# Performance work log

Measured on AMD Instinct MI355X. Metric: run time of the kernel, lower is better.

Reference implementation:

```python
import jax, jax.numpy as jnp
import numpy as np


def setup_inputs() -> dict:
    key = jax.random.key(0)
    k1, k2, k3 = jax.random.split(key, 3)
    B, S, E = 4, 8192, 1024
    x = jax.random.normal(k1, (B, S, E), dtype=jnp.float32)
    # torch nn.Linear weights have shape [out_features, in_features]
    W1 = jax.random.normal(k2, (3 * E, E), dtype=jnp.float32) * (1.0 / np.sqrt(E))
    W2 = jax.random.normal(k3, (E, E), dtype=jnp.float32) * (1.0 / np.sqrt(E))
    return {"x": x, "W1": W1, "W2": W2, "heads": 16}


def reference(x, W1, W2, heads):
    B, S, E = x.shape
    h = heads
    e = E // h
    # qkv projection: [B,S,3E] -> 'b s (n h e) -> n b h s e'
    qkv = (x @ W1.T).reshape(B, S, 3, h, e)
    qkv = jnp.transpose(qkv, (2, 0, 3, 1, 4))  # [3,B,h,S,e]
    q, k, v = qkv[0], qkv[1], qkv[2]
    # score: [B,h,e,e], softmax over last dim (c)
    score = jax.nn.softmax(jnp.einsum('bhnk,bhnc->bhkc', k / 4, v), axis=-1)
    # einsum 'bhnk,bhkc->bhnk': elementwise over k, sum over c
    attn = jax.nn.softmax(jnp.einsum('bhnk,bhkc->bhnk', q / 4, score), axis=-1)
    # 'b h s e -> b s (h e)' then linear_2
    out = jnp.transpose(attn, (0, 2, 1, 3)).reshape(B, S, E) @ W2.T
    return out
```

## Files before the change

kernel.cpp:

```cpp
#include <hip/hip_runtime.h>
#include <hip/hip_bf16.h>
#include <stdint.h>

static constexpr int MTOT = 32768;
static constexpr int KD   = 1024;
static constexpr int ND   = 1024;

static constexpr int BM = 256, BN = 256, BK = 64;
static constexpr int NT = KD / BK;
static constexpr int BUF_BYTES = 65536;
static constexpr int BOFF = 32768;
static constexpr int HALF = 16384;

typedef __bf16 bf16x8 __attribute__((ext_vector_type(8)));
typedef float  f32x4  __attribute__((ext_vector_type(4)));

__device__ __forceinline__ unsigned short f2bf_rne(float f) {
  union { float f; uint32_t u; } c; c.f = f;
  uint32_t u = c.u;
  return (unsigned short)((u + 0x7fffu + ((u >> 16) & 1u)) >> 16);
}

__global__ void cast_f32_to_bf16(const float* __restrict__ src,
                                 unsigned short* __restrict__ dst, int n4) {
  int idx = blockIdx.x * blockDim.x + threadIdx.x;
  int stride = gridDim.x * blockDim.x;
  for (int i = idx; i < n4; i += stride) {
    float4 v = reinterpret_cast<const float4*>(src)[i];
    ushort4 o;
    o.x = f2bf_rne(v.x); o.y = f2bf_rne(v.y);
    o.z = f2bf_rne(v.z); o.w = f2bf_rne(v.w);
    reinterpret_cast<ushort4*>(dst)[i] = o;
  }
}

__device__ __forceinline__ void gload_lds16(const void* g, void* lds) {
  __builtin_amdgcn_global_load_lds(
      (const __attribute__((address_space(1))) unsigned int*)g,
      (__attribute__((address_space(3))) unsigned int*)lds, 16, 0, 0);
}

template <int SOFTMAX>
__global__ __launch_bounds__(512, 2)
void gemm8(const unsigned short* __restrict__ A,
           const unsigned short* __restrict__ Bm,
           void* __restrict__ Cout) {
  extern __shared__ __align__(16) char ldsc[];

  const int tid  = threadIdx.x;
  const int lane = tid & 63;
  const int wid  = tid >> 6;
  const int wm = wid >> 2, wn = wid & 3;
  const int fr = lane & 15, fq = lane >> 4;

  const int bid0 = blockIdx.x;
  const int bid  = ((bid0 & 7) << 6) | (bid0 >> 3);
  const int brow = (bid >> 2) * BM;
  const int bcol = (bid & 3) * BN;

  const int srow  = tid >> 3;
  const int sslot = (tid & 7) ^ (srow & 7);
  const unsigned short* gA = A  + (size_t)(brow + srow) * KD + sslot * 8;
  const unsigned short* gB = Bm + (size_t)(bcol + srow) * KD + sslot * 8;

  f32x4  acc[8][4] = {};
  bf16x8 a0[4][2], a1[4][2], bA[2][2], bB[2][2];

  auto STAGE = [&](const unsigned short* g, int h, int kt, int b, int opOff) {
    const unsigned short* gu = g + (size_t)(h * 128) * KD + kt * BK;
    char* du = ldsc + b * BUF_BYTES + opOff + h * HALF + (wid << 10);
    gload_lds16(gu, du);
    gload_lds16(gu + (size_t)64 * KD, du + 8192);
  };

  auto rdA = [&](int b, bf16x8 (*dst)[2], int mBase) {
    const char* base = ldsc + b * BUF_BYTES + wm * HALF;
    #pragma unroll
    for (int mm = 0; mm < 4; ++mm) {
      const int r = (mBase + mm) * 16 + fr;
      #pragma unroll
      for (int ks = 0; ks < 2; ++ks)
        dst[mm][ks] = *(const bf16x8*)(base + (r << 7) +
                        ((ks * 64 + fq * 16) ^ ((r & 7) << 4)));
    }
  };
  auto rdB = [&](int b, int nBase, bf16x8 (*dst)[2]) {
    const char* base = ldsc + b * BUF_BYTES + BOFF + (wn >> 1) * HALF;
    #pragma unroll
    for (int nn = 0; nn < 2; ++nn) {
      const int r = (wn & 1) * 64 + (nBase + nn) * 16 + fr;
      #pragma unroll
      for (int ks = 0; ks < 2; ++ks)
        dst[nn][ks] = *(const bf16x8*)(base + (r << 7) +
                       ((ks * 64 + fq * 16) ^ ((r & 7) << 4)));
    }
  };
  auto MFMA16 = [&](int mBase, int nBase, bf16x8 (*af)[2], bf16x8 (*bf)[2]) {
    __builtin_amdgcn_s_setprio(1);
    #pragma unroll
    for (int ks = 0; ks < 2; ++ks)
      #pragma unroll
      for (int mm = 0; mm < 4; ++mm)
        #pragma unroll
        for (int nn = 0; nn < 2; ++nn)
          acc[mBase + mm][nBase + nn] = __builtin_amdgcn_mfma_f32_16x16x32_bf16(
              af[mm][ks], bf[nn][ks], acc[mBase + mm][nBase + nn], 0, 0, 0);
    __builtin_amdgcn_s_setprio(0);
  };

  auto tileStep = [&](int T, int cur, int nxt) {
    const int tp1 = (T + 1 < NT) ? T + 1 : NT - 1;
    const int tp2 = (T + 2 < NT) ? T + 2 : NT - 1;

    rdA(cur, a0, 0);
    rdA(cur, a1, 4);
    STAGE(gB, 0, tp1, nxt, BOFF);
    STAGE(gB, 1, tp1, nxt, BOFF);
    MFMA16(0, 0, a0, bA);

    MFMA16(4, 0, a1, bA);
    __builtin_amdgcn_s_barrier();

    rdB(cur, 2, bB);
    STAGE(gA, 0, tp2, cur, 0);
    MFMA16(4, 2, a1, bB);

    STAGE(gA, 1, tp2, cur, 0);
    asm volatile("s_waitcnt vmcnt(4)" ::: "memory");
    __builtin_amdgcn_s_barrier();
    rdB(nxt, 0, bA);
    MFMA16(0, 2, a0, bB);
    __builtin_amdgcn_s_barrier();
  };

  STAGE(gA, 0, 0, 0, 0);    STAGE(gA, 1, 0, 0, 0);
  STAGE(gB, 0, 0, 0, BOFF); STAGE(gB, 1, 0, 0, BOFF);
  STAGE(gA, 0, 1, 1, 0);    STAGE(gA, 1, 1, 1, 0);
  asm volatile("s_waitcnt vmcnt(4)" ::: "memory");
  __builtin_amdgcn_s_barrier();
  rdB(0, 0, bA);

  for (int T = 0; T < NT; T += 2) {
    tileStep(T,     0, 1);
    tileStep(T + 1, 1, 0);
  }

  if constexpr (SOFTMAX) {
    unsigned short* attn = reinterpret_cast<unsigned short*>(Cout);
    constexpr float CEXP = 0.25f * 1.44269504088896340736f;
    #pragma unroll
    for (int m = 0; m < 8; ++m) {
      const int row = brow + wm * 128 + m * 16 + fq * 4;
      #pragma unroll
      for (int j = 0; j < 4; ++j) {
        float v0 = acc[m][0][j], v1 = acc[m][1][j];
        float v2 = acc[m][2][j], v3 = acc[m][3][j];
        float mx = fmaxf(fmaxf(v0, v1), fmaxf(v2, v3));
        #pragma unroll
        for (int s = 1; s < 16; s <<= 1) mx = fmaxf(mx, __shfl_xor(mx, s, 64));
        float p0 = exp2f((v0 - mx) * CEXP);
        float p1 = exp2f((v1 - mx) * CEXP);
        float p2 = exp2f((v2 - mx) * CEXP);
        float p3 = exp2f((v3 - mx) * CEXP);
        float sm = p0 + p1 + p2 + p3;
        #pragma unroll
        for (int s = 1; s < 16; s <<= 1) sm += __shfl_xor(sm, s, 64);
        const float inv = 1.0f / sm;
        unsigned short* dst =
            attn + (size_t)(row + j) * ND + (bcol + wn * 64 + fr);
        dst[0]  = f2bf_rne(p0 * inv);
        dst[16] = f2bf_rne(p1 * inv);
        dst[32] = f2bf_rne(p2 * inv);
        dst[48] = f2bf_rne(p3 * inv);
      }
    }
  } else {
    float* Cf = reinterpret_cast<float*>(Cout);
    #pragma unroll
    for (int m = 0; m < 8; ++m) {
      const int row = brow + wm * 128 + m * 16 + fq * 4;
      #pragma unroll
      for (int n = 0; n < 4; ++n) {
        const int col = bcol + wn * 64 + n * 16 + fr;
        #pragma unroll
        for (int j = 0; j < 4; ++j)
          Cf[(size_t)(row + j) * ND + col] = acc[m][n][j];
      }
    }
  }
}

extern "C" void kernel_launch(void* const* d_in, const int* in_sizes, int n_in,
                              void* d_out, int out_size, void* d_ws, size_t ws_size,
                              hipStream_t stream) {
  const float* x  = (const float*)d_in[0];
  const float* W1 = (const float*)d_in[1];
  const float* W2 = (const float*)d_in[2];
  float* out = (float*)d_out;

  char* ws = (char*)d_ws;
  unsigned short* xb   = (unsigned short*)(ws);
  unsigned short* w1b  = (unsigned short*)(ws + (size_t)67108864);
  unsigned short* w2b  = (unsigned short*)(ws + (size_t)69206016);
  unsigned short* attn = (unsigned short*)(ws + (size_t)71303168);

  hipFuncSetAttribute(reinterpret_cast<const void*>(gemm8<1>),
                      hipFuncAttributeMaxDynamicSharedMemorySize, 131072);
  hipFuncSetAttribute(reinterpret_cast<const void*>(gemm8<0>),
                      hipFuncAttributeMaxDynamicSharedMemorySize, 131072);

  cast_f32_to_bf16<<<2048, 256, 0, stream>>>(x,  xb,  MTOT * KD / 4);
  cast_f32_to_bf16<<<512,  256, 0, stream>>>(W1, w1b, KD * KD / 4);
  cast_f32_to_bf16<<<512,  256, 0, stream>>>(W2, w2b, KD * KD / 4);

  const int nblk = (MTOT / BM) * (ND / BN);
  gemm8<1><<<nblk, 512, 131072, stream>>>(xb, w1b, (void*)attn);
  gemm8<0><<<nblk, 512, 131072, stream>>>(attn, w2b, (void*)out);
}
```

Before: 189.3 us.

## Load GEMM B-operand fragments directly from global into registers, halving LDS

```diff
diff --git a/kernel.cpp b/kernel.cpp
--- a/kernel.cpp
+++ b/kernel.cpp
@@ -8,8 +8,7 @@
 
 static constexpr int BM = 256, BN = 256, BK = 64;
 static constexpr int NT = KD / BK;
-static constexpr int BUF_BYTES = 65536;
-static constexpr int BOFF = 32768;
+static constexpr int BUF_BYTES = 32768;
 static constexpr int HALF = 16384;
 
 typedef __bf16 bf16x8 __attribute__((ext_vector_type(8)));
@@ -60,15 +59,14 @@
 
   const int srow  = tid >> 3;
   const int sslot = (tid & 7) ^ (srow & 7);
-  const unsigned short* gA = A  + (size_t)(brow + srow) * KD + sslot * 8;
-  const unsigned short* gB = Bm + (size_t)(bcol + srow) * KD + sslot * 8;
+  const unsigned short* gA = A + (size_t)(brow + srow) * KD + sslot * 8;
 
   f32x4  acc[8][4] = {};
   bf16x8 a0[4][2], a1[4][2], bA[2][2], bB[2][2];
 
-  auto STAGE = [&](const unsigned short* g, int h, int kt, int b, int opOff) {
-    const unsigned short* gu = g + (size_t)(h * 128) * KD + kt * BK;
-    char* du = ldsc + b * BUF_BYTES + opOff + h * HALF + (wid << 10);
+  auto STAGE = [&](int h, int kt, int b) {
+    const unsigned short* gu = gA + (size_t)(h * 128) * KD + kt * BK;
+    char* du = ldsc + b * BUF_BYTES + h * HALF + (wid << 10);
     gload_lds16(gu, du);
     gload_lds16(gu + (size_t)64 * KD, du + 8192);
   };
@@ -84,15 +82,13 @@
                         ((ks * 64 + fq * 16) ^ ((r & 7) << 4)));
     }
   };
-  auto rdB = [&](int b, int nBase, bf16x8 (*dst)[2]) {
-    const char* base = ldsc + b * BUF_BYTES + BOFF + (wn >> 1) * HALF;
+  auto gldB = [&](int kt, int nBase, bf16x8 (*dst)[2]) {
     #pragma unroll
     for (int nn = 0; nn < 2; ++nn) {
-      const int r = (wn & 1) * 64 + (nBase + nn) * 16 + fr;
+      const size_t r = (size_t)(bcol + wn * 64 + (nBase + nn) * 16 + fr);
       #pragma unroll
       for (int ks = 0; ks < 2; ++ks)
-        dst[nn][ks] = *(const bf16x8*)(base + (r << 7) +
-                       ((ks * 64 + fq * 16) ^ ((r & 7) << 4)));
+        dst[nn][ks] = *(const bf16x8*)(Bm + r * KD + kt * BK + ks * 32 + fq * 8);
     }
   };
   auto MFMA16 = [&](int mBase, int nBase, bf16x8 (*af)[2], bf16x8 (*bf)[2]) {
@@ -113,32 +109,29 @@
     const int tp2 = (T + 2 < NT) ? T + 2 : NT - 1;
 
     rdA(cur, a0, 0);
+    MFMA16(0, 0, a0, bA);
+
     rdA(cur, a1, 4);
-    STAGE(gB, 0, tp1, nxt, BOFF);
-    STAGE(gB, 1, tp1, nxt, BOFF);
-    MFMA16(0, 0, a0, bA);
-
+    gldB(T, 2, bB);
     MFMA16(4, 0, a1, bA);
     __builtin_amdgcn_s_barrier();
 
-    rdB(cur, 2, bB);
-    STAGE(gA, 0, tp2, cur, 0);
+    STAGE(0, tp2, cur);
     MFMA16(4, 2, a1, bB);
 
-    STAGE(gA, 1, tp2, cur, 0);
+    STAGE(1, tp2, cur);
     asm volatile("s_waitcnt vmcnt(4)" ::: "memory");
     __builtin_amdgcn_s_barrier();
-    rdB(nxt, 0, bA);
+    gldB(tp1, 0, bA);
     MFMA16(0, 2, a0, bB);
     __builtin_amdgcn_s_barrier();
   };
 
-  STAGE(gA, 0, 0, 0, 0);    STAGE(gA, 1, 0, 0, 0);
-  STAGE(gB, 0, 0, 0, BOFF); STAGE(gB, 1, 0, 0, BOFF);
-  STAGE(gA, 0, 1, 1, 0);    STAGE(gA, 1, 1, 1, 0);
+  gldB(0, 0, bA);
+  STAGE(0, 0, 0); STAGE(1, 0, 0);
+  STAGE(0, 1, 1); STAGE(1, 1, 1);
   asm volatile("s_waitcnt vmcnt(4)" ::: "memory");
   __builtin_amdgcn_s_barrier();
-  rdB(0, 0, bA);
 
   for (int T = 0; T < NT; T += 2) {
     tileStep(T,     0, 1);
@@ -205,15 +198,15 @@
   unsigned short* attn = (unsigned short*)(ws + (size_t)71303168);
 
   hipFuncSetAttribute(reinterpret_cast<const void*>(gemm8<1>),
-                      hipFuncAttributeMaxDynamicSharedMemorySize, 131072);
+                      hipFuncAttributeMaxDynamicSharedMemorySize, 65536);
   hipFuncSetAttribute(reinterpret_cast<const void*>(gemm8<0>),
-                      hipFuncAttributeMaxDynamicSharedMemorySize, 131072);
+                      hipFuncAttributeMaxDynamicSharedMemorySize, 65536);
 
   cast_f32_to_bf16<<<2048, 256, 0, stream>>>(x,  xb,  MTOT * KD / 4);
   cast_f32_to_bf16<<<512,  256, 0, stream>>>(W1, w1b, KD * KD / 4);
   cast_f32_to_bf16<<<512,  256, 0, stream>>>(W2, w2b, KD * KD / 4);
 
   const int nblk = (MTOT / BM) * (ND / BN);
-  gemm8<1><<<nblk, 512, 131072, stream>>>(xb, w1b, (void*)attn);
-  gemm8<0><<<nblk, 512, 131072, stream>>>(attn, w2b, (void*)out);
-}
+  gemm8<1><<<nblk, 512, 65536, stream>>>(xb, w1b, (void*)attn);
+  gemm8<0><<<nblk, 512, 65536, stream>>>(attn, w2b, (void*)out);
+}
```

After: 257.5 us. 36.0% more time.
